# Kernel optimization log

Hardware: AMD Instinct MI355X
Metric: run time of the kernel (lower is better)

## Reference

```python
import jax, jax.numpy as jnp
import numpy as np
from jax import lax

B, S, H = 20000, 1, 1
SPIN, TRAINLEN = 365, 15000
ML, SL = 2.9086, 1.898  # hard-coded PET normalization constants from source


def setup_inputs() -> dict:
    key = jax.random.key(0)
    ks = jax.random.split(key, 24)
    inp = {
        "x": jax.random.uniform(ks[0], (B, S, 2), jnp.float32),
        "y_obs": jax.random.uniform(ks[1], (B, 1), jnp.float32),
        "p_mean": jax.random.uniform(ks[2], (1,), jnp.float32),
        "p_std": jax.random.uniform(ks[3], (1,), jnp.float32),
        "epoch": 1,
        "time_lag": 0,
    }
    mat_names = ["weight_r_yom", "weight_r_yom_fp", "weight_r_yom_gw", "weight_r_ylm",
                 "weight_r_yfm", "weight_b1_yom", "weight_b1_yom_gw", "weight_b1_yom_fp",
                 "weight_b2_ylm", "theltaC"]
    vec_names = ["bias_b0_yom", "bias_b0_yom_gw", "bias_b0_yom_fp", "bias_b0_ylm"]
    for i, n in enumerate(mat_names):
        inp[n] = jax.random.uniform(ks[4 + i], (H, H), jnp.float32)
    for i, n in enumerate(vec_names):
        inp[n] = jax.random.uniform(ks[14 + i], (H,), jnp.float32)
    return inp


def _forward(x, y_obs, p_mean, p_std, weight_r_yom, weight_r_yom_fp, weight_r_yom_gw,
             weight_r_ylm, weight_r_yfm, bias_b0_yom, weight_b1_yom, bias_b0_yom_gw,
             weight_b1_yom_gw, bias_b0_yom_fp, weight_b1_yom_fp, bias_b0_ylm,
             weight_b2_ylm, theltaC, time_lag):
    relu, sig = jax.nn.relu, jax.nn.sigmoid
    tmap = jax.tree_util.tree_map
    # gate prefactors depend only on params -> hoisted out of the scan
    denom = (jnp.exp(weight_r_yom) + jnp.exp(weight_r_yom_gw) + jnp.exp(weight_r_ylm)
             + jnp.exp(weight_r_yfm) + jnp.exp(weight_r_yom_fp))
    oo1 = jnp.exp(weight_r_yom) / denom
    oogw1 = jnp.exp(weight_r_yom_gw) / denom
    oofp1 = jnp.exp(weight_r_yom_fp) / denom
    ol1 = jnp.exp(weight_r_ylm) / denom
    expC = jnp.exp(theltaC)
    mo, so = p_mean, p_std
    obsstd = jnp.std(y_obs[SPIN:TRAINLEN], ddof=1)  # torch.std is unbiased

    def gate_step(c0, u):
        u1 = u[0].reshape(1, 1)  # precip, broadcast to [1,H]
        u2 = u[1].reshape(1, 1)  # PET
        px = relu(u1 + c0 - expC)  # bypass/overflow flux
        ib = jnp.where(u1 > 0, px / jnp.where(u1 == 0, 1.0, u1), 0.0)
        z = (c0 - mo) / so
        oo = oo1 * sig(bias_b0_yom + z @ weight_b1_yom)
        oogw = oogw1 * sig(bias_b0_yom_gw + z @ weight_b1_yom_gw)
        oofp = oofp1 * sig(bias_b0_yom_fp + z @ weight_b1_yom_fp)
        ol = ol1 * sig(bias_b0_ylm + ((u2 - ML) / SL) @ weight_b2_ylm)
        olc = jnp.where(c0 > 0, ol - relu(ol - u2 / jnp.where(c0 > 0, c0, 1.0)), ol)
        f = 1.0 - oo - oofp - oogw - olc
        c1 = f * c0 + (u1 - px)  # mass-conserving state update
        outs = {"q": oo * c0, "h": oo * c0 + px, "hfp": oofp * c0, "c": c0,
                "l": ol * c0, "lc": olc * c0, "bp": px, "gw": oogw * c0,
                "ib": ib, "oo": oo, "ol": ol, "oofp": oofp, "f": f,
                "olc": olc, "oogw": oogw}
        return c1, outs

    def b_step(c0, binp):  # outer loop over 'batch' (acts as time axis)
        b, xb = binp
        c_fin, seq_outs = lax.scan(gate_step, c0, xb)  # xb: [S,2]
        outs = tmap(lambda a: a[-1], seq_outs)  # only last t survives the store
        active = b >= time_lag
        c_new = jnp.where(active, c_fin, c0)
        outs = tmap(lambda a: jnp.where(active, a, 0.0), outs)
        return c_new, outs

    nB = x.shape[0]
    c_init = jnp.zeros((1, H), x.dtype)
    _, O = lax.scan(b_step, c_init, (jnp.arange(nB), x))
    O = tmap(lambda a: a.reshape(nB, H), O)
    obs_std = jnp.where(jnp.arange(nB)[:, None] >= time_lag, obsstd, 0.0).astype(x.dtype)
    h_nout = jnp.concatenate([O["h"], obs_std], axis=1)
    return (O["h"], O["hfp"], O["c"], O["l"], O["lc"], O["bp"], O["gw"], O["ib"],
            O["oo"], O["oofp"], O["ol"], O["olc"], O["f"], O["oogw"], h_nout, obs_std)


def reference(x, y_obs, p_mean, p_std, epoch, time_lag, weight_r_yom, weight_r_yom_fp,
              weight_r_yom_gw, weight_r_ylm, weight_r_yfm, bias_b0_yom, weight_b1_yom,
              bias_b0_yom_gw, weight_b1_yom_gw, bias_b0_yom_fp, weight_b1_yom_fp,
              bias_b0_ylm, weight_b2_ylm, theltaC):
    return _forward(x, y_obs, p_mean, p_std, weight_r_yom, weight_r_yom_fp,
                    weight_r_yom_gw, weight_r_ylm, weight_r_yfm, bias_b0_yom,
                    weight_b1_yom, bias_b0_yom_gw, weight_b1_yom_gw, bias_b0_yom_fp,
                    weight_b1_yom_fp, bias_b0_ylm, weight_b2_ylm, theltaC, time_lag)
```

## Files before the change

### kernel.cpp

```cpp
#include <hip/hip_runtime.h>
#include <math.h>

#define NB 20000
#define SPIN 365
#define TRAINLEN 15000
#define ML_C 2.9086f
#define SL_C 1.898f

#define CHUNK 8
#define WSPEC 48
#define NLANES 2500
#define NSCANBLK 40
#define WIN 560
#define ROW 71

#define EX2(x) __builtin_amdgcn_exp2f(x)
#define RCP(x) __builtin_amdgcn_rcpf(x)
#define L2E 1.4426950408889634f

__global__ __launch_bounds__(64) void fused_kernel(
    const float* __restrict__ x, const float* __restrict__ y,
    const float* __restrict__ p_mean, const float* __restrict__ p_std,
    const int* __restrict__ time_lag,
    const float* __restrict__ w_r_yom, const float* __restrict__ w_r_yom_fp,
    const float* __restrict__ w_r_yom_gw, const float* __restrict__ w_r_ylm,
    const float* __restrict__ w_r_yfm,
    const float* __restrict__ w_b1_yom, const float* __restrict__ w_b1_yom_gw,
    const float* __restrict__ w_b1_yom_fp, const float* __restrict__ w_b2_ylm,
    const float* __restrict__ theltaC,
    const float* __restrict__ b0_yom, const float* __restrict__ b0_yom_gw,
    const float* __restrict__ b0_yom_fp, const float* __restrict__ b0_ylm,
    float* __restrict__ out) {
  const int lane = threadIdx.x;
  const int tl = time_lag[0];

  if (blockIdx.x == NSCANBLK) {
    double a = 0.0, q = 0.0;
    if (lane < 3) {
      double v = (double)y[SPIN + lane];
      a += v; q += v * v;
    }
    const float4* y4 = (const float4*)(y + 368);
    for (int i = lane; i < 3658; i += 64) {
      float4 v = y4[i];
      double v0 = v.x, v1 = v.y, v2 = v.z, v3 = v.w;
      a += v0 + v1 + v2 + v3;
      q += v0 * v0 + v1 * v1 + v2 * v2 + v3 * v3;
    }
    for (int off = 32; off > 0; off >>= 1) {
      a += __shfl_xor(a, off, 64);
      q += __shfl_xor(q, off, 64);
    }
    const double n = (double)(TRAINLEN - SPIN);
    const float sd = (float)sqrt((q - a * a / n) / (n - 1.0));
    for (int i = lane; i < NB / 4; i += 64) {
      int t = 4 * i;
      float4 v;
      v.x = (t >= tl) ? sd : 0.f;
      v.y = (t + 1 >= tl) ? sd : 0.f;
      v.z = (t + 2 >= tl) ? sd : 0.f;
      v.w = (t + 3 >= tl) ? sd : 0.f;
      *(float4*)(out + 16 * NB + t) = v;
    }
    for (int t = lane; t < NB; t += 64)
      out[14 * NB + 2 * t + 1] = (t >= tl) ? sd : 0.f;
    return;
  }

  __shared__ float2 xs[8 * ROW];
  const float2* __restrict__ xv = (const float2*)x;
  const int wstart = blockIdx.x * (64 * CHUNK) - WSPEC;

  float2 stg[9];
#pragma unroll
  for (int r = 0; r < 9; ++r) {
    int g = wstart + r * 64 + lane;
    g = g < 0 ? 0 : (g > NB - 1 ? NB - 1 : g);
    if (r < 8 || lane < WIN - 512) stg[r] = xv[g];
  }

  float e1 = __expf(w_r_yom[0]);
  float e2 = __expf(w_r_yom_gw[0]);
  float e3 = __expf(w_r_ylm[0]);
  float e4 = __expf(w_r_yfm[0]);
  float e5 = __expf(w_r_yom_fp[0]);
  float rd = 1.f / (e1 + e2 + e3 + e4 + e5);
  float oo1 = e1 * rd, oogw1 = e2 * rd, oofp1 = e5 * rd, ol1 = e3 * rd;
  float expC = __expf(theltaC[0]);
  float mo = p_mean[0];
  float inv_so = 1.f / p_std[0];
  float w1 = w_b1_yom[0], w1gw = w_b1_yom_gw[0], w1fp = w_b1_yom_fp[0], w2 = w_b2_ylm[0];
  float k_oo = -L2E * (w1 * inv_so);
  float d_oo = -L2E * (b0_yom[0] - mo * inv_so * w1);
  float k_gw = -L2E * (w1gw * inv_so);
  float d_gw = -L2E * (b0_yom_gw[0] - mo * inv_so * w1gw);
  float k_fp = -L2E * (w1fp * inv_so);
  float d_fp = -L2E * (b0_yom_fp[0] - mo * inv_so * w1fp);
  float k_ol = -L2E * (w2 / SL_C);
  float d_ol = -L2E * (b0_ylm[0] - (ML_C / SL_C) * w2);
  const int tl0 = tl > 0 ? tl : 0;

#pragma unroll
  for (int r = 0; r < 9; ++r) {
    if (r < 8 || lane < WIN - 512)
      xs[(lane & 7) * ROW + (lane >> 3) + 8 * r] = stg[r];
  }
  __syncthreads();

  const int gid = blockIdx.x * 64 + lane;
  const int start = gid * CHUNK;
  const int begin = start - WSPEC;

  float c = 0.f;
  float2 cur = xs[lane];

#pragma unroll 1
  for (int t = 0; t < WSPEC; ++t) {
    const int tn = t + 1;
    float2 nxt = xs[((tn & 7) * ROW) + lane + (tn >> 3)];
    float u1 = cur.x, u2 = cur.y;
    float soo = RCP(1.f + EX2(fmaf(c, k_oo, d_oo)));
    float sgw = RCP(1.f + EX2(fmaf(c, k_gw, d_gw)));
    float sfp = RCP(1.f + EX2(fmaf(c, k_fp, d_fp)));
    float sol = RCP(1.f + EX2(fmaf(u2, k_ol, d_ol)));
    float oo = oo1 * soo, oogw = oogw1 * sgw, oofp = oofp1 * sfp;
    float ol = ol1 * sol;
    float ratio = u2 * RCP(c);
    float olc = (c > 0.f) ? fminf(ratio, ol) : ol;
    float px = fmaxf(u1 + c - expC, 0.f);
    float fg = 1.f - ((oo + oofp) + (oogw + olc));
    float cn = fmaf(fg, c, u1 - px);
    c = ((begin + t) >= tl0) ? cn : c;
    cur = nxt;
  }

  const bool w = (gid < NLANES);
  float* __restrict__ op = out + start;
#pragma unroll 1
  for (int k = 0; k < 8; ++k) {
    const int tn = WSPEC + k + 1;
    float2 nxt = xs[((tn & 7) * ROW) + lane + (tn >> 3)];
    float u1 = cur.x, u2 = cur.y;
    float px = fmaxf(u1 + c - expC, 0.f);
    float iu = (u1 > 0.f) ? RCP(u1) : 0.f;
    float ib = px * iu;
    float soo = RCP(1.f + EX2(fmaf(c, k_oo, d_oo)));
    float sgw = RCP(1.f + EX2(fmaf(c, k_gw, d_gw)));
    float sfp = RCP(1.f + EX2(fmaf(c, k_fp, d_fp)));
    float sol = RCP(1.f + EX2(fmaf(u2, k_ol, d_ol)));
    float oo = oo1 * soo, oogw = oogw1 * sgw, oofp = oofp1 * sfp, ol = ol1 * sol;
    float ratio = u2 * RCP(c);
    float olc = (c > 0.f) ? (ol - fmaxf(ol - ratio, 0.f)) : ol;
    float fg = 1.f - oo - oofp - oogw - olc;
    bool act = (start + k) >= tl0;
    float m = act ? 1.f : 0.f;
    float h = m * fmaf(oo, c, px);
    if (w) {
      op[0 * NB + k]  = h;
      op[1 * NB + k]  = m * (oofp * c);
      op[2 * NB + k]  = m * c;
      op[3 * NB + k]  = m * (ol * c);
      op[4 * NB + k]  = m * (olc * c);
      op[5 * NB + k]  = m * px;
      op[6 * NB + k]  = m * (oogw * c);
      op[7 * NB + k]  = m * ib;
      op[8 * NB + k]  = m * oo;
      op[9 * NB + k]  = m * oofp;
      op[10 * NB + k] = m * ol;
      op[11 * NB + k] = m * olc;
      op[12 * NB + k] = m * fg;
      op[13 * NB + k] = m * oogw;
      out[14 * NB + 2 * (start + k)] = h;
    }
    if (act) c = fmaf(fg, c, u1 - px);
    cur = nxt;
  }
}

extern "C" void kernel_launch(void* const* d_in, const int* in_sizes, int n_in,
                              void* d_out, int out_size, void* d_ws, size_t ws_size,
                              hipStream_t stream) {
  const float* x        = (const float*)d_in[0];
  const float* y_obs    = (const float*)d_in[1];
  const float* p_mean   = (const float*)d_in[2];
  const float* p_std    = (const float*)d_in[3];
  const int* time_lag   = (const int*)d_in[5];
  const float* w_r_yom    = (const float*)d_in[6];
  const float* w_r_yom_fp = (const float*)d_in[7];
  const float* w_r_yom_gw = (const float*)d_in[8];
  const float* w_r_ylm    = (const float*)d_in[9];
  const float* w_r_yfm    = (const float*)d_in[10];
  const float* w_b1_yom   = (const float*)d_in[11];
  const float* w_b1_yom_gw= (const float*)d_in[12];
  const float* w_b1_yom_fp= (const float*)d_in[13];
  const float* w_b2_ylm   = (const float*)d_in[14];
  const float* theltaC    = (const float*)d_in[15];
  const float* b0_yom     = (const float*)d_in[16];
  const float* b0_yom_gw  = (const float*)d_in[17];
  const float* b0_yom_fp  = (const float*)d_in[18];
  const float* b0_ylm     = (const float*)d_in[19];
  float* out = (float*)d_out;
  (void)d_ws; (void)ws_size;

  fused_kernel<<<NSCANBLK + 1, 64, 0, stream>>>(
      x, y_obs, p_mean, p_std, time_lag,
      w_r_yom, w_r_yom_fp, w_r_yom_gw, w_r_ylm, w_r_yfm,
      w_b1_yom, w_b1_yom_gw, w_b1_yom_fp, w_b2_ylm,
      theltaC, b0_yom, b0_yom_gw, b0_yom_fp, b0_ylm,
      out);
}
```

Measured before the change: 118.6 us.

## Replicate obs-std reduction in every scan block and drop dedicated reduction block

Removes the separate 41st block that computed the y_obs standard deviation and wrote the obs_std outputs. Every scan block now computes the reduction itself, using unrolled double-buffered float4 loads with split accumulators, and writes h_nout pairs as float2 along with obs_std alongside its own outputs. This avoids a serial straggler block and merges the strided stores, at the cost of 40x redundant reads of y and extra double-precision work in front of each block's recurrence.

After: 103.5 us. 12.8% less time.

```diff
diff --git a/kernel.cpp b/kernel.cpp
--- a/kernel.cpp
+++ b/kernel.cpp
@@ -33,39 +33,7 @@
     float* __restrict__ out) {
   const int lane = threadIdx.x;
   const int tl = time_lag[0];
-
-  if (blockIdx.x == NSCANBLK) {
-    double a = 0.0, q = 0.0;
-    if (lane < 3) {
-      double v = (double)y[SPIN + lane];
-      a += v; q += v * v;
-    }
-    const float4* y4 = (const float4*)(y + 368);
-    for (int i = lane; i < 3658; i += 64) {
-      float4 v = y4[i];
-      double v0 = v.x, v1 = v.y, v2 = v.z, v3 = v.w;
-      a += v0 + v1 + v2 + v3;
-      q += v0 * v0 + v1 * v1 + v2 * v2 + v3 * v3;
-    }
-    for (int off = 32; off > 0; off >>= 1) {
-      a += __shfl_xor(a, off, 64);
-      q += __shfl_xor(q, off, 64);
-    }
-    const double n = (double)(TRAINLEN - SPIN);
-    const float sd = (float)sqrt((q - a * a / n) / (n - 1.0));
-    for (int i = lane; i < NB / 4; i += 64) {
-      int t = 4 * i;
-      float4 v;
-      v.x = (t >= tl) ? sd : 0.f;
-      v.y = (t + 1 >= tl) ? sd : 0.f;
-      v.z = (t + 2 >= tl) ? sd : 0.f;
-      v.w = (t + 3 >= tl) ? sd : 0.f;
-      *(float4*)(out + 16 * NB + t) = v;
-    }
-    for (int t = lane; t < NB; t += 64)
-      out[14 * NB + 2 * t + 1] = (t >= tl) ? sd : 0.f;
-    return;
-  }
+  const int tl0 = tl > 0 ? tl : 0;
 
   __shared__ float2 xs[8 * ROW];
   const float2* __restrict__ xv = (const float2*)x;
@@ -78,6 +46,44 @@
     g = g < 0 ? 0 : (g > NB - 1 ? NB - 1 : g);
     if (r < 8 || lane < WIN - 512) stg[r] = xv[g];
   }
+
+  double a0 = 0.0, a1 = 0.0, q0 = 0.0, q1 = 0.0;
+  if (lane < 3) {
+    double v = (double)y[SPIN + lane];
+    a0 += v; q0 += v * v;
+  }
+  const float4* __restrict__ y4 = (const float4*)(y + 368);
+#define YACC(bv)                                                      \
+  {                                                                   \
+    double v0 = (bv).x, v1 = (bv).y, v2 = (bv).z, v3 = (bv).w;        \
+    a0 += v0 + v1; a1 += v2 + v3;                                     \
+    q0 += v0 * v0 + v1 * v1; q1 += v2 * v2 + v3 * v3;                 \
+  }
+  float4 ba[8], bb[8];
+#pragma unroll
+  for (int u = 0; u < 8; ++u) ba[u] = y4[lane + u * 64];
+#pragma unroll 1
+  for (int r = 0; r < 6; r += 2) {
+#pragma unroll
+    for (int u = 0; u < 8; ++u) bb[u] = y4[lane + (r + 1) * 512 + u * 64];
+#pragma unroll
+    for (int u = 0; u < 8; ++u) YACC(ba[u])
+#pragma unroll
+    for (int u = 0; u < 8; ++u) ba[u] = y4[lane + (r + 2) * 512 + u * 64];
+#pragma unroll
+    for (int u = 0; u < 8; ++u) YACC(bb[u])
+  }
+#pragma unroll
+  for (int u = 0; u < 8; ++u) YACC(ba[u])
+  { float4 v = y4[lane + 3584]; YACC(v) }
+  if (lane < 10) { float4 v = y4[lane + 3648]; YACC(v) }
+  double a = a0 + a1, q = q0 + q1;
+  for (int off = 32; off > 0; off >>= 1) {
+    a += __shfl_xor(a, off, 64);
+    q += __shfl_xor(q, off, 64);
+  }
+  const double n = (double)(TRAINLEN - SPIN);
+  const float sd = (float)sqrt((q - a * a / n) / (n - 1.0));
 
   float e1 = __expf(w_r_yom[0]);
   float e2 = __expf(w_r_yom_gw[0]);
@@ -98,7 +104,6 @@
   float d_fp = -L2E * (b0_yom_fp[0] - mo * inv_so * w1fp);
   float k_ol = -L2E * (w2 / SL_C);
   float d_ol = -L2E * (b0_ylm[0] - (ML_C / SL_C) * w2);
-  const int tl0 = tl > 0 ? tl : 0;
 
 #pragma unroll
   for (int r = 0; r < 9; ++r) {
@@ -155,6 +160,7 @@
     bool act = (start + k) >= tl0;
     float m = act ? 1.f : 0.f;
     float h = m * fmaf(oo, c, px);
+    float sv = ((start + k) >= tl) ? sd : 0.f;
     if (w) {
       op[0 * NB + k]  = h;
       op[1 * NB + k]  = m * (oofp * c);
@@ -170,7 +176,8 @@
       op[11 * NB + k] = m * olc;
       op[12 * NB + k] = m * fg;
       op[13 * NB + k] = m * oogw;
-      out[14 * NB + 2 * (start + k)] = h;
+      *(float2*)(out + 14 * NB + 2 * (start + k)) = make_float2(h, sv);
+      out[16 * NB + start + k] = sv;
     }
     if (act) c = fmaf(fg, c, u1 - px);
     cur = nxt;
@@ -202,7 +209,7 @@
   float* out = (float*)d_out;
   (void)d_ws; (void)ws_size;
 
-  fused_kernel<<<NSCANBLK + 1, 64, 0, stream>>>(
+  fused_kernel<<<NSCANBLK, 64, 0, stream>>>(
       x, y_obs, p_mean, p_std, time_lag,
       w_r_yom, w_r_yom_fp, w_r_yom_gw, w_r_ylm, w_r_yfm,
       w_b1_yom, w_b1_yom_gw, w_b1_yom_fp, w_b2_ylm,
```
